# Performance work log

Measured on AMD Instinct MI355X. Metric: run time of the kernel, lower is better.

## Reference

```python
import jax, jax.numpy as jnp
import numpy as np

B, T, DM, H, DK, DV = 2, 2048, 1024, 16, 64, 64


def setup_inputs() -> dict:
    key = jax.random.key(0)
    k = jax.random.split(key, 7)
    std_k = np.float32(1.0 / np.sqrt(DK))
    std_v = np.float32(1.0 / np.sqrt(DV))
    return {
        "xq": jax.random.normal(k[0], (B, T, DM), jnp.float32),
        "xk": jax.random.normal(k[1], (B, T, DM), jnp.float32),
        "xv": jax.random.normal(k[2], (B, T, DM), jnp.float32),
        "mask": jnp.ones((B, T), jnp.float32),  # padding mask: 1 = keep
        "w_q": jax.random.normal(k[3], (H, DM, DK), jnp.float32) * std_k,
        "w_k": jax.random.normal(k[4], (H, DM, DK), jnp.float32) * std_k,
        "w_v": jax.random.normal(k[5], (H, DM, DV), jnp.float32) * std_v,
        "w_o": jax.random.normal(k[6], (H * DV, DM), jnp.float32) * np.float32(1.0 / np.sqrt(H * DV)),
        "b_o": jnp.zeros((DM,), jnp.float32),
    }


def reference(xq, xk, xv, mask, w_q, w_k, w_v, w_o, b_o):
    d_k = w_q.shape[-1]
    # per-head projections: [B,T,DM] x [H,DM,DK] -> [B,H,T,DK]
    q = jnp.einsum('bsd,hdk->bhsk', xq, w_q)
    kk = jnp.einsum('btd,hdk->bhtk', xk, w_k)
    v = jnp.einsum('btd,hdv->bhtv', xv, w_v)
    # NOTE: source divides by d_k (not sqrt(d_k)) -- kept faithful
    scores = jnp.einsum('bhsk,bhtk->bhst', q, kk) / jnp.float32(d_k)
    # _padding_mask: multiply by mask broadcast over key dim, then any exact
    # zero (masked OR coincidentally zero score) becomes -inf -- kept faithful
    masked = scores * mask[:, None, None, :]
    scores = jnp.where(masked == 0.0, -jnp.inf, masked)
    attn = jax.nn.softmax(scores, axis=-1)
    out = jnp.einsum('bhst,bhtv->bhsv', attn, v)  # [B,H,T,DV]
    b, h, t, dv = out.shape
    concat = out.transpose(0, 2, 1, 3).reshape(b, t, h * dv)
    return concat @ w_o + b_o
```

## Files before the change

kernel.cpp:

```cpp
#include <hip/hip_runtime.h>
#include <hip/hip_bf16.h>


typedef __attribute__((ext_vector_type(8))) short short8;
typedef __attribute__((ext_vector_type(4))) short short4v;
typedef __attribute__((ext_vector_type(4))) float f32x4;
typedef __attribute__((ext_vector_type(4))) int i32x4;

__device__ __forceinline__ short f2bf(float f) {
  union { float f; unsigned u; } v; v.f = f;
  unsigned r = v.u + 0x7FFFu + ((v.u >> 16) & 1u);
  return (short)(r >> 16);
}

#define GLD_LDS(g, l) __builtin_amdgcn_global_load_lds( \
    (const __attribute__((address_space(1))) void*)(g), \
    (__attribute__((address_space(3))) void*)(l), 16, 0, 0)

__global__ __launch_bounds__(256) void prep_all(
    const float* __restrict__ xq, const float* __restrict__ xk,
    const float* __restrict__ xv, const float* __restrict__ wq,
    const float* __restrict__ wk, const float* __restrict__ wv,
    const float* __restrict__ wo,
    short* __restrict__ Xb, short* __restrict__ Wall, short* __restrict__ Wot)
{
  const int bx = blockIdx.x, tid = threadIdx.x;
  __shared__ float Lt[64][65];
  if (bx < 6144) {
    int z = bx >> 11;
    const float* x = z == 0 ? xq : (z == 1 ? xk : xv);
    size_t i = ((size_t)(bx & 2047) * 256 + tid) * 8;
    f32x4 f0 = *(const f32x4*)(x + i);
    f32x4 f1 = *(const f32x4*)(x + i + 4);
    short8 s;
#pragma unroll
    for (int j = 0; j < 4; j++) { s[j] = f2bf(f0[j]); s[4 + j] = f2bf(f1[j]); }
    *(short8*)(Xb + (size_t)z * 4194304 + i) = s;
  } else if (bx < 6912) {
    int bz = bx - 6144;
    int z = bz >> 8, inner = bz & 255;
    const float* w = z == 0 ? wq : (z == 1 ? wk : wv);
    short* Wt = Wall + (size_t)z * 1048576;
    int h = inner >> 4, d0 = (inner & 15) * 64;
#pragma unroll
    for (int it = 0; it < 4; it++) {
      int e = tid + it * 256;
      int dl = e >> 4, k4 = (e & 15) * 4;
      f32x4 v = *(const f32x4*)(w + ((size_t)(h * 1024 + d0 + dl) * 64) + k4);
#pragma unroll
      for (int j = 0; j < 4; j++) Lt[dl][k4 + j] = v[j];
    }
    __syncthreads();
#pragma unroll
    for (int it = 0; it < 4; it++) {
      int e = tid + it * 256;
      int kl = e >> 4, dq = e & 15;
      short4v s;
#pragma unroll
      for (int j = 0; j < 4; j++) s[j] = f2bf(Lt[dq * 4 + j][kl]);
      *(short4v*)(Wt + (size_t)(h * 64 + kl) * 1024 + d0 + dq * 4) = s;
    }
  } else {
    int bz = bx - 6912;
    int k0 = (bz >> 4) * 64, n0 = (bz & 15) * 64;
#pragma unroll
    for (int it = 0; it < 4; it++) {
      int e = tid + it * 256;
      int kl = e >> 4, n4 = (e & 15) * 4;
      f32x4 v = *(const f32x4*)(wo + (size_t)(k0 + kl) * 1024 + n0 + n4);
#pragma unroll
      for (int j = 0; j < 4; j++) Lt[kl][n4 + j] = v[j];
    }
    __syncthreads();
#pragma unroll
    for (int it = 0; it < 4; it++) {
      int e = tid + it * 256;
      int nl = e >> 4, kq = e & 15;
      short4v s;
#pragma unroll
      for (int j = 0; j < 4; j++) s[j] = f2bf(Lt[kq * 4 + j][nl]);
      *(short4v*)(Wot + (size_t)(n0 + nl) * 1024 + k0 + kq * 4) = s;
    }
  }
}

__global__ __launch_bounds__(256) void proj_qkv2(
    const short* __restrict__ Xb, const short* __restrict__ Wall,
    short* __restrict__ Qb, short* __restrict__ Kt2, short* __restrict__ Vt2)
{
  const int z = blockIdx.z;
  const short* X  = Xb   + (size_t)z * 4194304;
  const short* Wt = Wall + (size_t)z * 1048576;

  const int t0 = blockIdx.x * 128;
  const int n0 = blockIdx.y * 128;
  const int tid = threadIdx.x, w = tid >> 6, lane = tid & 63;
  const int c = lane & 15, q4 = lane >> 4;
  const int wn = (w & 1) * 64, wt = (w >> 1) * 64;
  const int srow = lane >> 2, scol = (lane & 3) * 8;

  __shared__ __align__(16) short Al[128 * 32];
  __shared__ __align__(16) short Bl[128 * 32];

  f32x4 acc[4][4] = {};

  for (int k0 = 0; k0 < 1024; k0 += 32) {
#pragma unroll
    for (int i = 0; i < 2; i++) {
      int rg = (w * 2 + i) * 16;
      GLD_LDS(Wt + (size_t)(n0 + rg + srow) * 1024 + k0 + scol, Al + rg * 32);
      GLD_LDS(X  + (size_t)(t0 + rg + srow) * 1024 + k0 + scol, Bl + rg * 32);
    }
    __syncthreads();
    short8 a[4], bfr[4];
#pragma unroll
    for (int i = 0; i < 4; i++)
      a[i] = *(const short8*)(Al + (wn + i * 16 + c) * 32 + q4 * 8);
#pragma unroll
    for (int j = 0; j < 4; j++)
      bfr[j] = *(const short8*)(Bl + (wt + j * 16 + c) * 32 + q4 * 8);
#pragma unroll
    for (int i = 0; i < 4; i++)
#pragma unroll
      for (int j = 0; j < 4; j++)
        acc[i][j] = __builtin_amdgcn_mfma_f32_16x16x32_bf16(a[i], bfr[j], acc[i][j], 0, 0, 0);
    __syncthreads();
  }

#pragma unroll
  for (int i = 0; i < 4; i++)
#pragma unroll
    for (int j = 0; j < 4; j++) {
      int n = n0 + wn + i * 16 + q4 * 4;
      int trow = t0 + wt + j * 16 + c;
      int b = trow >> 11, t = trow & 2047;
      int h = n >> 6, cc = n & 63;
      int bh = b * 16 + h;
      f32x4 v = acc[i][j];
      short4v pk;
#pragma unroll
      for (int r = 0; r < 4; r++) pk[r] = f2bf(v[r]);
      if (z == 0) {
        *(short4v*)(Qb + (size_t)(bh * 2048 + t) * 64 + cc) = pk;
      } else if (z == 1) {
        int t5 = t & 31, s_ = t5 >> 4, c_ = t5 & 15;
        size_t base = (size_t)bh * 131072 + (t >> 5) * 2048;
#pragma unroll
        for (int r = 0; r < 4; r++) {
          int dv = cc + r;
          Kt2[base + ((s_ * 2 + (dv >> 5)) * 16 + c_) * 32 + ((dv >> 3) & 3) * 8 + (dv & 7)] = pk[r];
        }
      } else {
        int t5 = t & 31;
        int kp = ((t5 >> 2) & 3) * 8 + ((t5 >> 4) & 1) * 4 + (t5 & 3);
        size_t base = (size_t)bh * 131072 + (t >> 5) * 2048;
#pragma unroll
        for (int r = 0; r < 4; r++)
          Vt2[base + (size_t)(cc + r) * 32 + kp] = pk[r];
      }
    }
}

__global__ __launch_bounds__(256, 2) void attn5(
    const short* __restrict__ Qb, const short* __restrict__ Kt2,
    const short* __restrict__ Vt2, const float* __restrict__ mask,
    short* __restrict__ AO)
{
  const int tblk = blockIdx.x;
  const int bh = blockIdx.y;
  const int b = bh >> 4, h = bh & 15;
  const short* Qh = Qb  + (size_t)bh * 131072;
  const short* Kh = Kt2 + (size_t)bh * 131072;
  const short* Vh = Vt2 + (size_t)bh * 131072;

  const int tid = threadIdx.x, w = tid >> 6, lane = tid & 63;
  const int c = lane & 15, q4 = lane >> 4;
  const int qrow0 = tblk * 128 + w * 32;

  short8 qa[2][2];
#pragma unroll
  for (int u = 0; u < 2; u++)
#pragma unroll
    for (int dc = 0; dc < 2; dc++)
      qa[u][dc] = *(const short8*)(Qh + (size_t)(qrow0 + u * 16 + c) * 64 + dc * 32 + q4 * 8);

  f32x4 acc[2][4] = {};
  float l[2] = {0.f, 0.f};
  const float LOG2E_64 = 1.44269504088896f * 0.015625f;

  const short* kP = Kh + c * 32 + q4 * 8;
  const short* vP = Vh + c * 32 + q4 * 8;
  const float* mP = mask + b * 2048 + q4 * 4;

  short8 kf0[2][2], kf1[2][2], va0[4], va1[4];

#define PREF(KF, VA) do { \
    KF[0][0] = *(const short8*)(kP);        KF[0][1] = *(const short8*)(kP + 512); \
    KF[1][0] = *(const short8*)(kP + 1024); KF[1][1] = *(const short8*)(kP + 1536); \
    VA[0] = *(const short8*)(vP);        VA[1] = *(const short8*)(vP + 512); \
    VA[2] = *(const short8*)(vP + 1024); VA[3] = *(const short8*)(vP + 1536); \
    kP += 2048; vP += 2048; \
  } while (0)

#define BODY(KF, VA) do { \
    f32x4 st[2][2] = {}; \
    _Pragma("unroll") \
    for (int u = 0; u < 2; u++) \
      _Pragma("unroll") \
      for (int s = 0; s < 2; s++) { \
        st[u][s] = __builtin_amdgcn_mfma_f32_16x16x32_bf16(KF[s][0], qa[u][0], st[u][s], 0, 0, 0); \
        st[u][s] = __builtin_amdgcn_mfma_f32_16x16x32_bf16(KF[s][1], qa[u][1], st[u][s], 0, 0, 0); \
      } \
    f32x4 cm[2], cb[2]; \
    _Pragma("unroll") \
    for (int s = 0; s < 2; s++) { \
      f32x4 mk = *(const f32x4*)(mP + s * 16); \
      cm[s] = mk * LOG2E_64; \
      cb[s] = (mk - 1.0f) * 240.0f; \
    } \
    mP += 32; \
    _Pragma("unroll") \
    for (int u = 0; u < 2; u++) { \
      unsigned pkd[2][2]; \
      _Pragma("unroll") \
      for (int s = 0; s < 2; s++) { \
        float e0 = __builtin_amdgcn_exp2f(st[u][s][0] * cm[s][0] + cb[s][0]); \
        float e1 = __builtin_amdgcn_exp2f(st[u][s][1] * cm[s][1] + cb[s][1]); \
        float e2 = __builtin_amdgcn_exp2f(st[u][s][2] * cm[s][2] + cb[s][2]); \
        float e3 = __builtin_amdgcn_exp2f(st[u][s][3] * cm[s][3] + cb[s][3]); \
        l[u] += (e0 + e1) + (e2 + e3); \
        union { float f; unsigned u; } a0, a1, a2, a3; \
        a0.f = e0; a1.f = e1; a2.f = e2; a3.f = e3; \
        pkd[s][0] = __builtin_amdgcn_perm(a1.u + 0x8000u, a0.u + 0x8000u, 0x07060302u); \
        pkd[s][1] = __builtin_amdgcn_perm(a3.u + 0x8000u, a2.u + 0x8000u, 0x07060302u); \
      } \
      union { i32x4 i; short8 s; } pb; \
      pb.i[0] = (int)pkd[0][0]; pb.i[1] = (int)pkd[0][1]; \
      pb.i[2] = (int)pkd[1][0]; pb.i[3] = (int)pkd[1][1]; \
      _Pragma("unroll") \
      for (int vs = 0; vs < 4; vs++) \
        acc[u][vs] = __builtin_amdgcn_mfma_f32_16x16x32_bf16(VA[vs], pb.s, acc[u][vs], 0, 0, 0); \
    } \
  } while (0)

  PREF(kf0, va0);
  for (int ii = 0; ii < 32; ii++) {
    PREF(kf1, va1);
    BODY(kf0, va0);
    if (ii < 31) PREF(kf0, va0);
    BODY(kf1, va1);
  }
#undef PREF
#undef BODY

#pragma unroll
  for (int u = 0; u < 2; u++) {
    float lu = l[u];
    lu += __shfl_xor(lu, 16);
    lu += __shfl_xor(lu, 32);
    float inv = 1.0f / lu;
    size_t row = (size_t)b * 2048 + qrow0 + u * 16 + c;
#pragma unroll
    for (int vs = 0; vs < 4; vs++) {
      f32x4 v = acc[u][vs];
      short4v pk;
#pragma unroll
      for (int r = 0; r < 4; r++) pk[r] = f2bf(v[r] * inv);
      *(short4v*)(AO + row * 1024 + h * 64 + vs * 16 + q4 * 4) = pk;
    }
  }
}

__global__ __launch_bounds__(256) void out_proj2(
    const short* __restrict__ AO, const short* __restrict__ Wot,
    const float* __restrict__ bo, float* __restrict__ out)
{
  const int t0 = blockIdx.x * 128;
  const int n0 = blockIdx.y * 128;
  const int tid = threadIdx.x, w = tid >> 6, lane = tid & 63;
  const int c = lane & 15, q4 = lane >> 4;
  const int wn = (w & 1) * 64, wt = (w >> 1) * 64;
  const int srow = lane >> 2, scol = (lane & 3) * 8;

  __shared__ __align__(16) short Al[128 * 32];
  __shared__ __align__(16) short Bl[128 * 32];

  f32x4 acc[4][4] = {};

  for (int k0 = 0; k0 < 1024; k0 += 32) {
#pragma unroll
    for (int i = 0; i < 2; i++) {
      int rg = (w * 2 + i) * 16;
      GLD_LDS(Wot + (size_t)(n0 + rg + srow) * 1024 + k0 + scol, Al + rg * 32);
      GLD_LDS(AO  + (size_t)(t0 + rg + srow) * 1024 + k0 + scol, Bl + rg * 32);
    }
    __syncthreads();
    short8 a[4], bfr[4];
#pragma unroll
    for (int i = 0; i < 4; i++)
      a[i] = *(const short8*)(Al + (wn + i * 16 + c) * 32 + q4 * 8);
#pragma unroll
    for (int j = 0; j < 4; j++)
      bfr[j] = *(const short8*)(Bl + (wt + j * 16 + c) * 32 + q4 * 8);
#pragma unroll
    for (int i = 0; i < 4; i++)
#pragma unroll
      for (int j = 0; j < 4; j++)
        acc[i][j] = __builtin_amdgcn_mfma_f32_16x16x32_bf16(a[i], bfr[j], acc[i][j], 0, 0, 0);
    __syncthreads();
  }

#pragma unroll
  for (int i = 0; i < 4; i++)
#pragma unroll
    for (int j = 0; j < 4; j++) {
      int n = n0 + wn + i * 16 + q4 * 4;
      int trow = t0 + wt + j * 16 + c;
      f32x4 v = acc[i][j] + *(const f32x4*)(bo + n);
      *(f32x4*)(out + (size_t)trow * 1024 + n) = v;
    }
}

extern "C" void kernel_launch(void* const* d_in, const int* in_sizes, int n_in,
                              void* d_out, int out_size, void* d_ws, size_t ws_size,
                              hipStream_t stream)
{
  (void)in_sizes; (void)n_in; (void)out_size; (void)ws_size;
  const float* xq   = (const float*)d_in[0];
  const float* xk   = (const float*)d_in[1];
  const float* xv   = (const float*)d_in[2];
  const float* mask = (const float*)d_in[3];
  const float* wq   = (const float*)d_in[4];
  const float* wk   = (const float*)d_in[5];
  const float* wv   = (const float*)d_in[6];
  const float* wo   = (const float*)d_in[7];
  const float* bo   = (const float*)d_in[8];
  float* out = (float*)d_out;

  char* ws = (char*)d_ws;
  short* Wall = (short*)(ws + (size_t)0);
  short* Wot  = (short*)(ws + ((size_t)6 << 20));
  short* Xb   = (short*)(ws + ((size_t)8 << 20));
  short* AO   = (short*)(ws + ((size_t)8 << 20));
  short* Qb   = (short*)(ws + ((size_t)32 << 20));
  short* Kt2  = (short*)(ws + ((size_t)40 << 20));
  short* Vt2  = (short*)(ws + ((size_t)48 << 20));

  prep_all<<<7168, 256, 0, stream>>>(xq, xk, xv, wq, wk, wv, wo, Xb, Wall, Wot);
  proj_qkv2<<<dim3(32, 8, 3), 256, 0, stream>>>(Xb, Wall, Qb, Kt2, Vt2);
  attn5<<<dim3(16, 32), 256, 0, stream>>>(Qb, Kt2, Vt2, mask, AO);
  out_proj2<<<dim3(32, 8), 256, 0, stream>>>(AO, Wot, bo, out);
}
```

Measured before the change: 243.8 us.

## Use single-wave attention blocks with 64 query rows and vectorize K/V stores

The attention kernel moves from 4-wave blocks of 32 rows per wave to 1-wave blocks covering 64 query rows, doubling how often each loaded K/V fragment is reused. K is prefetched one step ahead, V is loaded inline, and the grid doubles to compensate. The QKV projection swaps MFMA operand order for V so its transposed layout can be written with vector short4 stores, and K stores are also vectorized. This reduces global traffic and scattered scalar stores, at the cost of higher register pressure and fewer waves per block.

```diff
diff --git a/kernel.cpp b/kernel.cpp
--- a/kernel.cpp
+++ b/kernel.cpp
@@ -119,11 +119,19 @@
 #pragma unroll
     for (int j = 0; j < 4; j++)
       bfr[j] = *(const short8*)(Bl + (wt + j * 16 + c) * 32 + q4 * 8);
-#pragma unroll
-    for (int i = 0; i < 4; i++)
-#pragma unroll
-      for (int j = 0; j < 4; j++)
-        acc[i][j] = __builtin_amdgcn_mfma_f32_16x16x32_bf16(a[i], bfr[j], acc[i][j], 0, 0, 0);
+    if (z == 2) {
+#pragma unroll
+      for (int i = 0; i < 4; i++)
+#pragma unroll
+        for (int j = 0; j < 4; j++)
+          acc[i][j] = __builtin_amdgcn_mfma_f32_16x16x32_bf16(bfr[j], a[i], acc[i][j], 0, 0, 0);
+    } else {
+#pragma unroll
+      for (int i = 0; i < 4; i++)
+#pragma unroll
+        for (int j = 0; j < 4; j++)
+          acc[i][j] = __builtin_amdgcn_mfma_f32_16x16x32_bf16(a[i], bfr[j], acc[i][j], 0, 0, 0);
+    }
     __syncthreads();
   }
 
@@ -131,37 +139,39 @@
   for (int i = 0; i < 4; i++)
 #pragma unroll
     for (int j = 0; j < 4; j++) {
-      int n = n0 + wn + i * 16 + q4 * 4;
-      int trow = t0 + wt + j * 16 + c;
-      int b = trow >> 11, t = trow & 2047;
-      int h = n >> 6, cc = n & 63;
-      int bh = b * 16 + h;
       f32x4 v = acc[i][j];
       short4v pk;
 #pragma unroll
       for (int r = 0; r < 4; r++) pk[r] = f2bf(v[r]);
       if (z == 0) {
-        *(short4v*)(Qb + (size_t)(bh * 2048 + t) * 64 + cc) = pk;
+        int n = n0 + wn + i * 16 + q4 * 4;
+        int trow = t0 + wt + j * 16 + c;
+        int b = trow >> 11, t = trow & 2047;
+        int h = n >> 6, cc = n & 63;
+        *(short4v*)(Qb + (size_t)((b * 16 + h) * 2048 + t) * 64 + cc) = pk;
       } else if (z == 1) {
+        int n = n0 + wn + i * 16 + q4 * 4;
+        int trow = t0 + wt + j * 16 + c;
+        int b = trow >> 11, t = trow & 2047;
+        int h = n >> 6, cc = n & 63;
         int t5 = t & 31, s_ = t5 >> 4, c_ = t5 & 15;
-        size_t base = (size_t)bh * 131072 + (t >> 5) * 2048;
-#pragma unroll
-        for (int r = 0; r < 4; r++) {
-          int dv = cc + r;
-          Kt2[base + ((s_ * 2 + (dv >> 5)) * 16 + c_) * 32 + ((dv >> 3) & 3) * 8 + (dv & 7)] = pk[r];
-        }
+        size_t base = (size_t)(b * 16 + h) * 131072 + (t >> 5) * 2048;
+        *(short4v*)(Kt2 + base + ((s_ * 2 + (cc >> 5)) * 16 + c_) * 32
+                        + ((cc >> 3) & 3) * 8 + (cc & 7)) = pk;
       } else {
+        int dv = n0 + wn + i * 16 + c;
+        int trow = t0 + wt + j * 16 + q4 * 4;
+        int b = trow >> 11, t = trow & 2047;
+        int h = dv >> 6, cc = dv & 63;
         int t5 = t & 31;
-        int kp = ((t5 >> 2) & 3) * 8 + ((t5 >> 4) & 1) * 4 + (t5 & 3);
-        size_t base = (size_t)bh * 131072 + (t >> 5) * 2048;
-#pragma unroll
-        for (int r = 0; r < 4; r++)
-          Vt2[base + (size_t)(cc + r) * 32 + kp] = pk[r];
+        int kp = ((t5 >> 2) & 3) * 8 + ((t5 >> 4) & 1) * 4;
+        size_t base = (size_t)(b * 16 + h) * 131072 + (t >> 5) * 2048;
+        *(short4v*)(Vt2 + base + (size_t)cc * 32 + kp) = pk;
       }
     }
 }
 
-__global__ __launch_bounds__(256, 2) void attn5(
+__global__ __launch_bounds__(64, 2) void attn6(
     const short* __restrict__ Qb, const short* __restrict__ Kt2,
     const short* __restrict__ Vt2, const float* __restrict__ mask,
     short* __restrict__ AO)
@@ -173,44 +183,47 @@
   const short* Kh = Kt2 + (size_t)bh * 131072;
   const short* Vh = Vt2 + (size_t)bh * 131072;
 
-  const int tid = threadIdx.x, w = tid >> 6, lane = tid & 63;
+  const int lane = threadIdx.x & 63;
   const int c = lane & 15, q4 = lane >> 4;
-  const int qrow0 = tblk * 128 + w * 32;
-
-  short8 qa[2][2];
-#pragma unroll
-  for (int u = 0; u < 2; u++)
+  const int qrow0 = tblk * 64;
+
+  short8 qa[4][2];
+#pragma unroll
+  for (int u = 0; u < 4; u++)
 #pragma unroll
     for (int dc = 0; dc < 2; dc++)
       qa[u][dc] = *(const short8*)(Qh + (size_t)(qrow0 + u * 16 + c) * 64 + dc * 32 + q4 * 8);
 
-  f32x4 acc[2][4] = {};
-  float l[2] = {0.f, 0.f};
+  f32x4 acc[4][4] = {};
+  float l[4] = {0.f, 0.f, 0.f, 0.f};
   const float LOG2E_64 = 1.44269504088896f * 0.015625f;
 
   const short* kP = Kh + c * 32 + q4 * 8;
   const short* vP = Vh + c * 32 + q4 * 8;
   const float* mP = mask + b * 2048 + q4 * 4;
 
-  short8 kf0[2][2], kf1[2][2], va0[4], va1[4];
-
-#define PREF(KF, VA) do { \
-    KF[0][0] = *(const short8*)(kP);        KF[0][1] = *(const short8*)(kP + 512); \
-    KF[1][0] = *(const short8*)(kP + 1024); KF[1][1] = *(const short8*)(kP + 1536); \
-    VA[0] = *(const short8*)(vP);        VA[1] = *(const short8*)(vP + 512); \
-    VA[2] = *(const short8*)(vP + 1024); VA[3] = *(const short8*)(vP + 1536); \
-    kP += 2048; vP += 2048; \
+  short8 kf0[4], kf1[4], va[4];
+
+#define PREF_K(KF) do { \
+    KF[0] = *(const short8*)(kP);        KF[1] = *(const short8*)(kP + 512); \
+    KF[2] = *(const short8*)(kP + 1024); KF[3] = *(const short8*)(kP + 1536); \
+    kP += 2048; \
   } while (0)
 
-#define BODY(KF, VA) do { \
-    f32x4 st[2][2] = {}; \
+#define BODY(KF, KFN, doPref) do { \
+    va[0] = *(const short8*)(vP);        va[1] = *(const short8*)(vP + 512); \
+    va[2] = *(const short8*)(vP + 1024); va[3] = *(const short8*)(vP + 1536); \
+    vP += 2048; \
+    f32x4 st[4][2]; \
     _Pragma("unroll") \
-    for (int u = 0; u < 2; u++) \
+    for (int u = 0; u < 4; u++) \
       _Pragma("unroll") \
       for (int s = 0; s < 2; s++) { \
-        st[u][s] = __builtin_amdgcn_mfma_f32_16x16x32_bf16(KF[s][0], qa[u][0], st[u][s], 0, 0, 0); \
-        st[u][s] = __builtin_amdgcn_mfma_f32_16x16x32_bf16(KF[s][1], qa[u][1], st[u][s], 0, 0, 0); \
+        f32x4 z0 = {}; \
+        z0 = __builtin_amdgcn_mfma_f32_16x16x32_bf16(KF[s * 2], qa[u][0], z0, 0, 0, 0); \
+        st[u][s] = __builtin_amdgcn_mfma_f32_16x16x32_bf16(KF[s * 2 + 1], qa[u][1], z0, 0, 0, 0); \
       } \
+    if (doPref) PREF_K(KFN); \
     f32x4 cm[2], cb[2]; \
     _Pragma("unroll") \
     for (int s = 0; s < 2; s++) { \
@@ -220,7 +233,7 @@
     } \
     mP += 32; \
     _Pragma("unroll") \
-    for (int u = 0; u < 2; u++) { \
+    for (int u = 0; u < 4; u++) { \
       unsigned pkd[2][2]; \
       _Pragma("unroll") \
       for (int s = 0; s < 2; s++) { \
@@ -239,22 +252,20 @@
       pb.i[2] = (int)pkd[1][0]; pb.i[3] = (int)pkd[1][1]; \
       _Pragma("unroll") \
       for (int vs = 0; vs < 4; vs++) \
-        acc[u][vs] = __builtin_amdgcn_mfma_f32_16x16x32_bf16(VA[vs], pb.s, acc[u][vs], 0, 0, 0); \
+        acc[u][vs] = __builtin_amdgcn_mfma_f32_16x16x32_bf16(va[vs], pb.s, acc[u][vs], 0, 0, 0); \
     } \
   } while (0)
 
-  PREF(kf0, va0);
+  PREF_K(kf0);
   for (int ii = 0; ii < 32; ii++) {
-    PREF(kf1, va1);
-    BODY(kf0, va0);
-    if (ii < 31) PREF(kf0, va0);
-    BODY(kf1, va1);
-  }
-#undef PREF
+    BODY(kf0, kf1, 1);
+    BODY(kf1, kf0, ii < 31);
+  }
+#undef PREF_K
 #undef BODY
 
 #pragma unroll
-  for (int u = 0; u < 2; u++) {
+  for (int u = 0; u < 4; u++) {
     float lu = l[u];
     lu += __shfl_xor(lu, 16);
     lu += __shfl_xor(lu, 32);
@@ -348,6 +359,6 @@
 
   prep_all<<<7168, 256, 0, stream>>>(xq, xk, xv, wq, wk, wv, wo, Xb, Wall, Wot);
   proj_qkv2<<<dim3(32, 8, 3), 256, 0, stream>>>(Xb, Wall, Qb, Kt2, Vt2);
-  attn5<<<dim3(16, 32), 256, 0, stream>>>(Qb, Kt2, Vt2, mask, AO);
+  attn6<<<dim3(32, 32), 64, 0, stream>>>(Qb, Kt2, Vt2, mask, AO);
   out_proj2<<<dim3(32, 8), 256, 0, stream>>>(AO, Wot, bo, out);
 }
```

New measurement: 257.0 us. 5.4% more time.
